# Kernel tuning notes

Measured on AMD Instinct MI355X. Metric: run time of the kernel, lower is better.

Reference implementation:

```python
import jax, jax.numpy as jnp
import numpy as np

N = 50000
IN_C, HID_C, OUT_C = 512, 64, 40
E = 800000

def setup_inputs() -> dict:
    key = jax.random.key(0)
    ks = jax.random.split(key, 6)
    x = jax.random.normal(ks[0], (N, IN_C), dtype=jnp.float32)
    edge_index = jax.random.randint(ks[1], (2, E), 0, N, dtype=jnp.int64)
    # Glorot-style init for GCNConv linear weights, zero bias (PyG default)
    W1 = jax.random.normal(ks[2], (IN_C, HID_C), dtype=jnp.float32) / np.sqrt(IN_C)
    b1 = jnp.zeros((HID_C,), dtype=jnp.float32)
    W2 = jax.random.normal(ks[3], (HID_C, OUT_C), dtype=jnp.float32) / np.sqrt(HID_C)
    b2 = jnp.zeros((OUT_C,), dtype=jnp.float32)
    return {"x": x, "edge_index": edge_index, "W1": W1, "b1": b1, "W2": W2, "b2": b2}

def _gcn_conv(x, src, dst, W, b, n_nodes):
    # Standard GCNConv (self-loops already appended to src/dst):
    # h = x @ W; out[dst] += D^-1/2[src] * D^-1/2[dst] * h[src]; out += b
    h = x @ W
    deg = jnp.zeros((n_nodes,), dtype=h.dtype).at[dst].add(1.0)
    dinv = jnp.where(deg > 0, deg ** -0.5, 0.0)
    norm = dinv[src] * dinv[dst]                       # [E+N]
    msg = h[src] * norm[:, None]                       # gather + scale
    out = jax.ops.segment_sum(msg, dst, num_segments=n_nodes)
    return out + b

def reference(x, edge_index, W1, b1, W2, b2):
    n_nodes = x.shape[0]
    # add self-loops (PyG GCNConv default add_self_loops=True)
    loop = jnp.arange(n_nodes, dtype=edge_index.dtype)
    src = jnp.concatenate([edge_index[0], loop])
    dst = jnp.concatenate([edge_index[1], loop])
    # eval mode: dropout is identity
    h = _gcn_conv(x, src, dst, W1, b1, n_nodes)
    h = jax.nn.relu(h)
    h = _gcn_conv(h, src, dst, W2, b2, n_nodes)
    return jax.nn.softmax(h, axis=-1)
```

## Files before the change

kernel.cpp:

```cpp
#include <hip/hip_runtime.h>
#include <math.h>

#define IN_C 512
#define HID  64
#define OUTC 40

typedef __attribute__((ext_vector_type(8))) short bf16x8;
typedef __attribute__((ext_vector_type(4))) float f32x4;

#define GDEPTH 16

__device__ __forceinline__ ushort f2bf(float f) {
    uint u = __float_as_uint(f);
    u += 0x7FFFu + ((u >> 16) & 1u);
    return (ushort)(u >> 16);
}
__device__ __forceinline__ float bf2f(ushort s) {
    return __uint_as_float(((uint)s) << 16);
}

__device__ __forceinline__ void gl_lds16(const void* g, void* l) {
    __builtin_amdgcn_global_load_lds(
        (const __attribute__((address_space(1))) void*)g,
        (__attribute__((address_space(3))) void*)l,
        16, 0, 0);
}

__global__ void k_zero(int4* __restrict__ p, int n4) {
    int i = blockIdx.x * blockDim.x + threadIdx.x;
    if (i < n4) p[i] = make_int4(0, 0, 0, 0);
}

__global__ void k_histsplit(const int* __restrict__ dst, int E,
                            int* __restrict__ cnt, int* __restrict__ rank,
                            int nbE2,
                            const float* __restrict__ W,
                            ushort* __restrict__ hi, ushort* __restrict__ lo) {
    if (blockIdx.x < (unsigned)nbE2) {
        int i = (blockIdx.x * blockDim.x + threadIdx.x) * 2;
        if (i < E) {
            if (i + 1 < E) {
                int2 d = *(const int2*)&dst[i];
                int r0 = atomicAdd(&cnt[d.x], 1);
                int r1 = atomicAdd(&cnt[d.y], 1);
                *(int2*)&rank[i] = make_int2(r0, r1);
            } else {
                rank[i] = atomicAdd(&cnt[dst[i]], 1);
            }
        }
    } else {
        int i = (blockIdx.x - nbE2) * blockDim.x + threadIdx.x;
        if (i >= HID * IN_C) return;
        int c = i >> 9, k = i & 511;
        float v = W[(size_t)k * HID + c];
        uint ub = __float_as_uint(v);
        uint hb = ub & 0xFFFF0000u;
        float lf = v - __uint_as_float(hb);
        int lb = c * 64 + (k & 31) * 2;
        int pb = lb ^ (((lb >> 6) & 7) << 4);
        int pidx = (k >> 5) * 2048 + (pb >> 1);
        hi[pidx] = (ushort)(ub >> 16);
        lo[pidx] = (ushort)(__float_as_uint(lf) >> 16);
    }
}

__global__ void k_scan1(const int* __restrict__ cnt, int N,
                        int* __restrict__ rowptr, int* __restrict__ bsum) {
    __shared__ int s[256];
    int t = threadIdx.x;
    int i = blockIdx.x * 256 + t;
    int v = (i < N) ? cnt[i] : 0;
    int x = v;
    s[t] = x; __syncthreads();
    #pragma unroll
    for (int o = 1; o < 256; o <<= 1) {
        int y = (t >= o) ? s[t - o] : 0;
        __syncthreads();
        x += y; s[t] = x;
        __syncthreads();
    }
    if (i < N) rowptr[i] = x - v;
    if (t == 255) bsum[blockIdx.x] = x;
}

__global__ void k_scan23(int* __restrict__ rowptr, const int* __restrict__ bsum,
                         const int* __restrict__ cnt, float* __restrict__ dinv,
                         int N, int E, int nb) {
    __shared__ int s[256];
    int t = threadIdx.x;
    int v = (t < nb) ? bsum[t] : 0;
    int x = v;
    s[t] = x; __syncthreads();
    #pragma unroll
    for (int o = 1; o < 256; o <<= 1) {
        int y = (t >= o) ? s[t - o] : 0;
        __syncthreads();
        x += y; s[t] = x;
        __syncthreads();
    }
    int bpre = (blockIdx.x > 0) ? s[blockIdx.x - 1] : 0;
    int i = blockIdx.x * 256 + t;
    if (i < N) {
        rowptr[i] += bpre;
        dinv[i] = rsqrtf(1.0f + (float)cnt[i]);
        if (i == 0) rowptr[N] = E;
    }
}

__global__ __launch_bounds__(256) void k_gemm1fill(
        const float* __restrict__ x,
        const ushort* __restrict__ Bphi, const ushort* __restrict__ Bplo,
        const float* __restrict__ dinv, ushort* __restrict__ h1s,
        int N, int nbG,
        const int* __restrict__ src, const int* __restrict__ dst,
        const int* __restrict__ rank, int E,
        const int* __restrict__ rowptr, int* __restrict__ ssort) {
    __shared__ float  Af[2][2048];
    __shared__ ushort Bh[2][2048], Bl[2][2048];

    if (blockIdx.x >= (unsigned)nbG) {
        int i = ((blockIdx.x - nbG) * blockDim.x + threadIdx.x) * 2;
        if (i >= E) return;
        if (i + 1 < E) {
            int2 d = *(const int2*)&dst[i];
            int2 s = *(const int2*)&src[i];
            int2 r = *(const int2*)&rank[i];
            ssort[rowptr[d.x] + r.x] = s.x;
            ssort[rowptr[d.y] + r.y] = s.y;
        } else {
            ssort[rowptr[dst[i]] + rank[i]] = src[i];
        }
        return;
    }

    int t = threadIdx.x;
    int wid = t >> 6, lane = t & 63;
    int lr = lane & 15, lko = lane >> 4;
    int wm = wid >> 1, wn = wid & 1;
    int row0 = blockIdx.x * 64;

    int p0 = (wid * 64 + lane) * 16;
    int r0l = p0 >> 7;
    int o0 = p0 ^ ((r0l & 7) << 4);
    int g0 = row0 + r0l; if (g0 >= N) g0 = N - 1;
    const char* xsrc0 = (const char*)x + (size_t)g0 * 2048 + (o0 & 127);
    int p1 = p0 + 4096;
    int r1l = p1 >> 7;
    int o1 = p1 ^ ((r1l & 7) << 4);
    int g1 = row0 + r1l; if (g1 >= N) g1 = N - 1;
    const char* xsrc1 = (const char*)x + (size_t)g1 * 2048 + (o1 & 127);
    const char* bsrcH = (const char*)Bphi + (size_t)(wid * 64 + lane) * 16;
    const char* bsrcL = (const char*)Bplo + (size_t)(wid * 64 + lane) * 16;

    f32x4 acc[2][2] = {};

    auto stage = [&](int tile, int b) {
        gl_lds16(xsrc0 + (size_t)tile * 128, (char*)&Af[b][0] + wid * 1024);
        gl_lds16(xsrc1 + (size_t)tile * 128, (char*)&Af[b][0] + 4096 + wid * 1024);
        gl_lds16(bsrcH + (size_t)tile * 4096, (char*)&Bh[b][0] + wid * 1024);
        gl_lds16(bsrcL + (size_t)tile * 4096, (char*)&Bl[b][0] + wid * 1024);
    };
    auto compute = [&](int b) {
        bf16x8 afh[2], afl[2], bfh[2], bfl[2];
        #pragma unroll
        for (int mf = 0; mf < 2; ++mf) {
            int row = wm * 32 + mf * 16 + lr;
            int fi = (row * 32 + lko * 8) ^ ((row & 7) << 2);
            f32x4 a0 = *(const f32x4*)&Af[b][fi];
            f32x4 a1 = *(const f32x4*)&Af[b][fi ^ 4];
            float av[8];
            *(f32x4*)&av[0] = a0;
            *(f32x4*)&av[4] = a1;
            #pragma unroll
            for (int j = 0; j < 8; ++j) {
                uint ub = __float_as_uint(av[j]);
                float hf = __uint_as_float(ub & 0xFFFF0000u);
                float lf = av[j] - hf;
                afh[mf][j] = (short)(ub >> 16);
                afl[mf][j] = (short)(__float_as_uint(lf) >> 16);
            }
        }
        #pragma unroll
        for (int nf = 0; nf < 2; ++nf) {
            int col = wn * 32 + nf * 16 + lr;
            int ci = (col * 32 + lko * 8) ^ ((col & 7) << 3);
            bfh[nf] = *(const bf16x8*)&Bh[b][ci];
            bfl[nf] = *(const bf16x8*)&Bl[b][ci];
        }
        #pragma unroll
        for (int mf = 0; mf < 2; ++mf)
            #pragma unroll
            for (int nf = 0; nf < 2; ++nf) {
                acc[mf][nf] = __builtin_amdgcn_mfma_f32_16x16x32_bf16(afh[mf], bfh[nf], acc[mf][nf], 0, 0, 0);
                acc[mf][nf] = __builtin_amdgcn_mfma_f32_16x16x32_bf16(afl[mf], bfh[nf], acc[mf][nf], 0, 0, 0);
                acc[mf][nf] = __builtin_amdgcn_mfma_f32_16x16x32_bf16(afh[mf], bfl[nf], acc[mf][nf], 0, 0, 0);
            }
    };

    stage(0, 0);
    __syncthreads();

    #pragma unroll
    for (int i = 0; i < 16; ++i) {
        if (i < 15) stage(i + 1, (i + 1) & 1);
        compute(i & 1);
        __syncthreads();
    }

    #pragma unroll
    for (int mf = 0; mf < 2; ++mf)
        #pragma unroll
        for (int r = 0; r < 4; ++r) {
            int orow = row0 + wm * 32 + mf * 16 + lko * 4 + r;
            if (orow < N) {
                float dv = dinv[orow];
                #pragma unroll
                for (int nf = 0; nf < 2; ++nf)
                    h1s[(size_t)orow * HID + wn * 32 + nf * 16 + lr] = f2bf(dv * acc[mf][nf][r]);
            }
        }
}

__global__ __launch_bounds__(256) void k_agg1g2(const ushort* __restrict__ h1s,
                                                const int* __restrict__ rowptr,
                                                const int* __restrict__ ssort,
                                                const float* __restrict__ dinv,
                                                const float* __restrict__ b1,
                                                const float* __restrict__ W2,
                                                ushort* __restrict__ h2s, int N) {
    __shared__ float wl[HID * OUTC];
    int t = threadIdx.x;
    #pragma unroll
    for (int q0 = 0; q0 < 3; ++q0) {
        int q = t + q0 * 256;
        if (q < 640) *(float4*)&wl[q * 4] = *(const float4*)&W2[q * 4];
    }
    __syncthreads();

    int lane = t & 63;
    int wq = t >> 6;
    int lc = lane < OUTC ? lane : 0;
    float bias = b1[lane];
    int nq = (N + 3) >> 2;

    for (int q = blockIdx.x; q < nq; q += gridDim.x) {
        int node = q * 4 + wq;
        if (node >= N) continue;
        float s0 = bf2f(h1s[(size_t)node * HID + lane]);
        float sv[GDEPTH];
        #pragma unroll
        for (int k = 0; k < GDEPTH; ++k) sv[k] = 0.f;
        int eu = __builtin_amdgcn_readfirstlane(rowptr[node]);
        int endu = __builtin_amdgcn_readfirstlane(rowptr[node + 1]);
        for (int e = eu; e < endu; e += GDEPTH) {
            int raw[GDEPTH];
            #pragma unroll
            for (int k = 0; k < GDEPTH; ++k) raw[k] = ssort[e + k];
            #pragma unroll
            for (int k = 0; k < GDEPTH; ++k) {
                int ix = (e + k < endu) ? raw[k] : raw[0];
                float v = bf2f(h1s[(size_t)ix * HID + lane]);
                sv[k] += (e + k < endu) ? v : 0.f;
            }
        }
        float s = s0;
        #pragma unroll
        for (int k = 0; k < GDEPTH; ++k) s += sv[k];
        float dv = dinv[node];
        float a = fmaxf(fmaf(dv, s, bias), 0.0f);
        float acc = 0.f;
        #pragma unroll
        for (int k = 0; k < HID; ++k) {
            float ak = __uint_as_float(__builtin_amdgcn_readlane(__float_as_uint(a), k));
            acc = fmaf(ak, wl[k * OUTC + lc], acc);
        }
        if (lane < OUTC) h2s[(size_t)node * OUTC + lane] = f2bf(dv * acc);
    }
}

__global__ __launch_bounds__(256) void k_agg2(const ushort* __restrict__ h2s,
                                              const int* __restrict__ rowptr,
                                              const int* __restrict__ ssort,
                                              const float* __restrict__ dinv,
                                              const float* __restrict__ b2,
                                              float* __restrict__ out, int N) {
    int lane = threadIdx.x & 63;
    int node = blockIdx.x * 4 + (threadIdx.x >> 6);
    if (node >= N) return;
    bool act = lane < OUTC;
    int lc = act ? lane : 0;
    float s0 = bf2f(h2s[(size_t)node * OUTC + lc]);
    float sv[GDEPTH];
    #pragma unroll
    for (int k = 0; k < GDEPTH; ++k) sv[k] = 0.f;
    int eu = __builtin_amdgcn_readfirstlane(rowptr[node]);
    int endu = __builtin_amdgcn_readfirstlane(rowptr[node + 1]);
    for (int e = eu; e < endu; e += GDEPTH) {
        int raw[GDEPTH];
        #pragma unroll
        for (int k = 0; k < GDEPTH; ++k) raw[k] = ssort[e + k];
        #pragma unroll
        for (int k = 0; k < GDEPTH; ++k) {
            int ix = (e + k < endu) ? raw[k] : raw[0];
            float v = bf2f(h2s[(size_t)ix * OUTC + lc]);
            sv[k] += (e + k < endu) ? v : 0.f;
        }
    }
    float s = s0;
    #pragma unroll
    for (int k = 0; k < GDEPTH; ++k) s += sv[k];
    float v = act ? (dinv[node] * s + b2[lane]) : -INFINITY;
    float m = v;
    #pragma unroll
    for (int o = 32; o; o >>= 1) m = fmaxf(m, __shfl_xor(m, o));
    float p = act ? expf(v - m) : 0.0f;
    float su = p;
    #pragma unroll
    for (int o = 32; o; o >>= 1) su += __shfl_xor(su, o);
    if (act) out[(size_t)node * OUTC + lane] = p / su;
}

static inline size_t alignup(size_t v) { return (v + 255) & ~(size_t)255; }

extern "C" void kernel_launch(void* const* d_in, const int* in_sizes, int n_in,
                              void* d_out, int out_size, void* d_ws, size_t ws_size,
                              hipStream_t stream) {
    const float* x  = (const float*)d_in[0];
    const int*   ei = (const int*)d_in[1];
    const float* W1 = (const float*)d_in[2];
    const float* b1 = (const float*)d_in[3];
    const float* W2 = (const float*)d_in[4];
    const float* b2 = (const float*)d_in[5];

    const int N = in_sizes[0] / IN_C;
    const int E = in_sizes[1] / 2;
    const int* src = ei;
    const int* dst = ei + E;

    char* w = (char*)d_ws;
    int* cnt    = (int*)w;   w += alignup((size_t)N * 4);
    int* rank   = (int*)w;   w += alignup((size_t)E * 4 + 256);
    int* rowptr = (int*)w;   w += alignup((size_t)(N + 1) * 4);
    int* bsum   = (int*)w;   w += alignup(256 * 4);
    int* ssort  = (int*)w;   w += alignup((size_t)E * 4 + 256);
    float* dinv = (float*)w; w += alignup((size_t)N * 4);
    ushort* h1s = (ushort*)w; w += alignup((size_t)N * HID * 2);
    ushort* h2s = (ushort*)w; w += alignup((size_t)N * OUTC * 2);
    ushort* Bphi = (ushort*)w; w += alignup((size_t)HID * IN_C * 2);
    ushort* Bplo = (ushort*)w; w += alignup((size_t)HID * IN_C * 2);

    const int n4 = (N + 3) / 4;
    k_zero<<<(n4 + 255) / 256, 256, 0, stream>>>((int4*)cnt, n4);

    const int nb   = (N + 255) / 256;
    const int nbE2 = (E / 2 + 255) / 256;
    const int nbW  = (HID * IN_C + 255) / 256;
    k_histsplit<<<nbE2 + nbW, 256, 0, stream>>>(dst, E, cnt, rank, nbE2, W1, Bphi, Bplo);
    k_scan1 <<<nb, 256, 0, stream>>>(cnt, N, rowptr, bsum);
    k_scan23<<<nb, 256, 0, stream>>>(rowptr, bsum, cnt, dinv, N, E, nb);

    const int nbG = (N + 63) / 64;
    k_gemm1fill<<<nbG + nbE2, 256, 0, stream>>>(x, Bphi, Bplo, dinv, h1s, N, nbG,
                                                src, dst, rank, E, rowptr, ssort);
    k_agg1g2<<<2048, 256, 0, stream>>>(h1s, rowptr, ssort, dinv, b1, W2, h2s, N);
    k_agg2  <<<(N + 3) / 4, 256, 0, stream>>>(h2s, rowptr, ssort, dinv, b2, (float*)d_out, N);
}
```

Baseline: 143.0 us.

## Split fill from GEMM1 and load full 32-row A tile into LDS upfront

The ssort fill pass is moved out of the fused GEMM launch into its own kernel. The first-layer GEMM now uses 32-row tiles and issues loads for the entire 32x512 fp32 A block into LDS at kernel start, so the K loop only double-buffers the small W1 hi/lo tiles. This issues all x traffic early for more memory-level parallelism, at the cost of 64KB+ of LDS per block, lower occupancy, one extra kernel launch and less per-wave MFMA reuse.

```diff
diff --git a/kernel.cpp b/kernel.cpp
--- a/kernel.cpp
+++ b/kernel.cpp
@@ -107,118 +107,101 @@
     }
 }
 
-__global__ __launch_bounds__(256) void k_gemm1fill(
+__global__ void k_fill(const int* __restrict__ src, const int* __restrict__ dst,
+                       const int* __restrict__ rank, int E,
+                       const int* __restrict__ rowptr, int* __restrict__ ssort) {
+    int i = (blockIdx.x * blockDim.x + threadIdx.x) * 2;
+    if (i >= E) return;
+    if (i + 1 < E) {
+        int2 d = *(const int2*)&dst[i];
+        int2 s = *(const int2*)&src[i];
+        int2 r = *(const int2*)&rank[i];
+        ssort[rowptr[d.x] + r.x] = s.x;
+        ssort[rowptr[d.y] + r.y] = s.y;
+    } else {
+        ssort[rowptr[dst[i]] + rank[i]] = src[i];
+    }
+}
+
+__global__ __launch_bounds__(256) void k_gemm1(
         const float* __restrict__ x,
         const ushort* __restrict__ Bphi, const ushort* __restrict__ Bplo,
-        const float* __restrict__ dinv, ushort* __restrict__ h1s,
-        int N, int nbG,
-        const int* __restrict__ src, const int* __restrict__ dst,
-        const int* __restrict__ rank, int E,
-        const int* __restrict__ rowptr, int* __restrict__ ssort) {
-    __shared__ float  Af[2][2048];
+        const float* __restrict__ dinv, ushort* __restrict__ h1s, int N) {
+    __shared__ float  Af[32 * 512];
     __shared__ ushort Bh[2][2048], Bl[2][2048];
-
-    if (blockIdx.x >= (unsigned)nbG) {
-        int i = ((blockIdx.x - nbG) * blockDim.x + threadIdx.x) * 2;
-        if (i >= E) return;
-        if (i + 1 < E) {
-            int2 d = *(const int2*)&dst[i];
-            int2 s = *(const int2*)&src[i];
-            int2 r = *(const int2*)&rank[i];
-            ssort[rowptr[d.x] + r.x] = s.x;
-            ssort[rowptr[d.y] + r.y] = s.y;
-        } else {
-            ssort[rowptr[dst[i]] + rank[i]] = src[i];
-        }
-        return;
-    }
 
     int t = threadIdx.x;
     int wid = t >> 6, lane = t & 63;
     int lr = lane & 15, lko = lane >> 4;
     int wm = wid >> 1, wn = wid & 1;
-    int row0 = blockIdx.x * 64;
-
-    int p0 = (wid * 64 + lane) * 16;
-    int r0l = p0 >> 7;
-    int o0 = p0 ^ ((r0l & 7) << 4);
-    int g0 = row0 + r0l; if (g0 >= N) g0 = N - 1;
-    const char* xsrc0 = (const char*)x + (size_t)g0 * 2048 + (o0 & 127);
-    int p1 = p0 + 4096;
-    int r1l = p1 >> 7;
-    int o1 = p1 ^ ((r1l & 7) << 4);
-    int g1 = row0 + r1l; if (g1 >= N) g1 = N - 1;
-    const char* xsrc1 = (const char*)x + (size_t)g1 * 2048 + (o1 & 127);
-    const char* bsrcH = (const char*)Bphi + (size_t)(wid * 64 + lane) * 16;
-    const char* bsrcL = (const char*)Bplo + (size_t)(wid * 64 + lane) * 16;
-
-    f32x4 acc[2][2] = {};
-
-    auto stage = [&](int tile, int b) {
-        gl_lds16(xsrc0 + (size_t)tile * 128, (char*)&Af[b][0] + wid * 1024);
-        gl_lds16(xsrc1 + (size_t)tile * 128, (char*)&Af[b][0] + 4096 + wid * 1024);
-        gl_lds16(bsrcH + (size_t)tile * 4096, (char*)&Bh[b][0] + wid * 1024);
-        gl_lds16(bsrcL + (size_t)tile * 4096, (char*)&Bl[b][0] + wid * 1024);
-    };
-    auto compute = [&](int b) {
-        bf16x8 afh[2], afl[2], bfh[2], bfl[2];
-        #pragma unroll
-        for (int mf = 0; mf < 2; ++mf) {
-            int row = wm * 32 + mf * 16 + lr;
-            int fi = (row * 32 + lko * 8) ^ ((row & 7) << 2);
-            f32x4 a0 = *(const f32x4*)&Af[b][fi];
-            f32x4 a1 = *(const f32x4*)&Af[b][fi ^ 4];
-            float av[8];
-            *(f32x4*)&av[0] = a0;
-            *(f32x4*)&av[4] = a1;
-            #pragma unroll
-            for (int j = 0; j < 8; ++j) {
-                uint ub = __float_as_uint(av[j]);
-                float hf = __uint_as_float(ub & 0xFFFF0000u);
-                float lf = av[j] - hf;
-                afh[mf][j] = (short)(ub >> 16);
-                afl[mf][j] = (short)(__float_as_uint(lf) >> 16);
-            }
-        }
+    int row0 = blockIdx.x * 32;
+
+    const char* xb = (const char*)x;
+    #pragma unroll
+    for (int j = 0; j < 16; ++j) {
+        int p = t * 16 + j * 4096;
+        int row = p >> 11;
+        int o = (p & 2047) ^ ((row & 7) << 4);
+        int grow = row0 + row; if (grow >= N) grow = N - 1;
+        gl_lds16(xb + (size_t)grow * 2048 + o, (char*)Af + j * 4096 + wid * 1024);
+    }
+    const char* bsrcH = (const char*)Bphi + (size_t)t * 16;
+    const char* bsrcL = (const char*)Bplo + (size_t)t * 16;
+    gl_lds16(bsrcH, (char*)&Bh[0][0] + wid * 1024);
+    gl_lds16(bsrcL, (char*)&Bl[0][0] + wid * 1024);
+    __syncthreads();
+
+    f32x4 acc[2] = {};
+
+    #pragma unroll
+    for (int i = 0; i < 16; ++i) {
+        if (i < 15) {
+            gl_lds16(bsrcH + (size_t)(i + 1) * 4096, (char*)&Bh[(i + 1) & 1][0] + wid * 1024);
+            gl_lds16(bsrcL + (size_t)(i + 1) * 4096, (char*)&Bl[(i + 1) & 1][0] + wid * 1024);
+        }
+        int row = wm * 16 + lr;
+        int fi = (row * 512 + i * 32 + lko * 8) ^ ((row & 7) << 2);
+        f32x4 a0 = *(const f32x4*)&Af[fi];
+        f32x4 a1 = *(const f32x4*)&Af[fi ^ 4];
+        float av[8];
+        *(f32x4*)&av[0] = a0;
+        *(f32x4*)&av[4] = a1;
+        bf16x8 ahi, alo;
+        #pragma unroll
+        for (int j = 0; j < 8; ++j) {
+            uint ub = __float_as_uint(av[j]);
+            float hf = __uint_as_float(ub & 0xFFFF0000u);
+            float lf = av[j] - hf;
+            ahi[j] = (short)(ub >> 16);
+            alo[j] = (short)(__float_as_uint(lf) >> 16);
+        }
+        bf16x8 bfh[2], bfl[2];
         #pragma unroll
         for (int nf = 0; nf < 2; ++nf) {
             int col = wn * 32 + nf * 16 + lr;
             int ci = (col * 32 + lko * 8) ^ ((col & 7) << 3);
-            bfh[nf] = *(const bf16x8*)&Bh[b][ci];
-            bfl[nf] = *(const bf16x8*)&Bl[b][ci];
-        }
-        #pragma unroll
-        for (int mf = 0; mf < 2; ++mf)
+            bfh[nf] = *(const bf16x8*)&Bh[i & 1][ci];
+            bfl[nf] = *(const bf16x8*)&Bl[i & 1][ci];
+        }
+        #pragma unroll
+        for (int nf = 0; nf < 2; ++nf) {
+            acc[nf] = __builtin_amdgcn_mfma_f32_16x16x32_bf16(ahi, bfh[nf], acc[nf], 0, 0, 0);
+            acc[nf] = __builtin_amdgcn_mfma_f32_16x16x32_bf16(alo, bfh[nf], acc[nf], 0, 0, 0);
+            acc[nf] = __builtin_amdgcn_mfma_f32_16x16x32_bf16(ahi, bfl[nf], acc[nf], 0, 0, 0);
+        }
+        __syncthreads();
+    }
+
+    #pragma unroll
+    for (int r = 0; r < 4; ++r) {
+        int orow = row0 + wm * 16 + lko * 4 + r;
+        if (orow < N) {
+            float dv = dinv[orow];
             #pragma unroll
-            for (int nf = 0; nf < 2; ++nf) {
-                acc[mf][nf] = __builtin_amdgcn_mfma_f32_16x16x32_bf16(afh[mf], bfh[nf], acc[mf][nf], 0, 0, 0);
-                acc[mf][nf] = __builtin_amdgcn_mfma_f32_16x16x32_bf16(afl[mf], bfh[nf], acc[mf][nf], 0, 0, 0);
-                acc[mf][nf] = __builtin_amdgcn_mfma_f32_16x16x32_bf16(afh[mf], bfl[nf], acc[mf][nf], 0, 0, 0);
-            }
-    };
-
-    stage(0, 0);
-    __syncthreads();
-
-    #pragma unroll
-    for (int i = 0; i < 16; ++i) {
-        if (i < 15) stage(i + 1, (i + 1) & 1);
-        compute(i & 1);
-        __syncthreads();
-    }
-
-    #pragma unroll
-    for (int mf = 0; mf < 2; ++mf)
-        #pragma unroll
-        for (int r = 0; r < 4; ++r) {
-            int orow = row0 + wm * 32 + mf * 16 + lko * 4 + r;
-            if (orow < N) {
-                float dv = dinv[orow];
-                #pragma unroll
-                for (int nf = 0; nf < 2; ++nf)
-                    h1s[(size_t)orow * HID + wn * 32 + nf * 16 + lr] = f2bf(dv * acc[mf][nf][r]);
-            }
-        }
+            for (int nf = 0; nf < 2; ++nf)
+                h1s[(size_t)orow * HID + wn * 32 + nf * 16 + lr] = f2bf(dv * acc[nf][r]);
+        }
+    }
 }
 
 __global__ __launch_bounds__(256) void k_agg1g2(const ushort* __restrict__ h1s,
@@ -358,10 +341,9 @@
     k_histsplit<<<nbE2 + nbW, 256, 0, stream>>>(dst, E, cnt, rank, nbE2, W1, Bphi, Bplo);
     k_scan1 <<<nb, 256, 0, stream>>>(cnt, N, rowptr, bsum);
     k_scan23<<<nb, 256, 0, stream>>>(rowptr, bsum, cnt, dinv, N, E, nb);
-
-    const int nbG = (N + 63) / 64;
-    k_gemm1fill<<<nbG + nbE2, 256, 0, stream>>>(x, Bphi, Bplo, dinv, h1s, N, nbG,
-                                                src, dst, rank, E, rowptr, ssort);
+    k_fill  <<<nbE2, 256, 0, stream>>>(src, dst, rank, E, rowptr, ssort);
+
+    k_gemm1 <<<(N + 31) / 32, 256, 0, stream>>>(x, Bphi, Bplo, dinv, h1s, N);
     k_agg1g2<<<2048, 256, 0, stream>>>(h1s, rowptr, ssort, dinv, b1, W2, h2s, N);
     k_agg2  <<<(N + 3) / 4, 256, 0, stream>>>(h2s, rowptr, ssort, dinv, b2, (float*)d_out, N);
 }
```

Measured after the change: 172.6 us. +20.7%, slower.

## Split layer-1 aggregation into two 32-channel halves for cache locality, separate GEMM2

Applied to the files above, without the earlier changes.

The first GEMM now writes the hidden features as two separate 32-channel arrays. Aggregation runs in two passes, one per half, so each gathered working set is half the size and more likely to stay in L2/MALL. The aggregated activation is written to a new buffer, and a separate kernel applies W2. This adds an extra kernel launch, an extra pass over the edge list, and an extra read and write of the activation buffer.

```diff
diff --git a/kernel.cpp b/kernel.cpp
--- a/kernel.cpp
+++ b/kernel.cpp
@@ -110,7 +110,8 @@
 __global__ __launch_bounds__(256) void k_gemm1fill(
         const float* __restrict__ x,
         const ushort* __restrict__ Bphi, const ushort* __restrict__ Bplo,
-        const float* __restrict__ dinv, ushort* __restrict__ h1s,
+        const float* __restrict__ dinv,
+        ushort* __restrict__ h1a, ushort* __restrict__ h1b,
         int N, int nbG,
         const int* __restrict__ src, const int* __restrict__ dst,
         const int* __restrict__ rank, int E,
@@ -207,6 +208,7 @@
         __syncthreads();
     }
 
+    ushort* hb = wn ? h1b : h1a;
     #pragma unroll
     for (int mf = 0; mf < 2; ++mf)
         #pragma unroll
@@ -216,16 +218,47 @@
                 float dv = dinv[orow];
                 #pragma unroll
                 for (int nf = 0; nf < 2; ++nf)
-                    h1s[(size_t)orow * HID + wn * 32 + nf * 16 + lr] = f2bf(dv * acc[mf][nf][r]);
+                    hb[(size_t)orow * 32 + nf * 16 + lr] = f2bf(dv * acc[mf][nf][r]);
             }
         }
 }
 
-__global__ __launch_bounds__(256) void k_agg1g2(const ushort* __restrict__ h1s,
-                                                const int* __restrict__ rowptr,
-                                                const int* __restrict__ ssort,
+__global__ __launch_bounds__(256) void k_aggh(const ushort* __restrict__ h1x,
+                                              const int* __restrict__ rowptr,
+                                              const int* __restrict__ ssort,
+                                              const float* __restrict__ dinv,
+                                              const float* __restrict__ b1,
+                                              ushort* __restrict__ a1f,
+                                              int N, int half) {
+    int t = blockIdx.x * blockDim.x + threadIdx.x;
+    int node = t >> 5;
+    int ch = t & 31;
+    if (node >= N) return;
+    float s0 = bf2f(h1x[(size_t)node * 32 + ch]);
+    float sv[GDEPTH];
+    #pragma unroll
+    for (int k = 0; k < GDEPTH; ++k) sv[k] = 0.f;
+    int elo = rowptr[node], ehi = rowptr[node + 1];
+    for (int e = elo; e < ehi; e += GDEPTH) {
+        int raw[GDEPTH];
+        #pragma unroll
+        for (int k = 0; k < GDEPTH; ++k) raw[k] = ssort[e + k];
+        #pragma unroll
+        for (int k = 0; k < GDEPTH; ++k) {
+            int ix = (e + k < ehi) ? raw[k] : raw[0];
+            float v = bf2f(h1x[(size_t)ix * 32 + ch]);
+            sv[k] += (e + k < ehi) ? v : 0.f;
+        }
+    }
+    float s = s0;
+    #pragma unroll
+    for (int k = 0; k < GDEPTH; ++k) s += sv[k];
+    float a = fmaxf(fmaf(dinv[node], s, b1[half * 32 + ch]), 0.0f);
+    __builtin_nontemporal_store(f2bf(a), &a1f[(size_t)node * 64 + half * 32 + ch]);
+}
+
+__global__ __launch_bounds__(256) void k_gemm2b(const ushort* __restrict__ a1f,
                                                 const float* __restrict__ dinv,
-                                                const float* __restrict__ b1,
                                                 const float* __restrict__ W2,
                                                 ushort* __restrict__ h2s, int N) {
     __shared__ float wl[HID * OUTC];
@@ -236,46 +269,18 @@
         if (q < 640) *(float4*)&wl[q * 4] = *(const float4*)&W2[q * 4];
     }
     __syncthreads();
-
     int lane = t & 63;
-    int wq = t >> 6;
+    int node = blockIdx.x * 4 + (t >> 6);
+    if (node >= N) return;
     int lc = lane < OUTC ? lane : 0;
-    float bias = b1[lane];
-    int nq = (N + 3) >> 2;
-
-    for (int q = blockIdx.x; q < nq; q += gridDim.x) {
-        int node = q * 4 + wq;
-        if (node >= N) continue;
-        float s0 = bf2f(h1s[(size_t)node * HID + lane]);
-        float sv[GDEPTH];
-        #pragma unroll
-        for (int k = 0; k < GDEPTH; ++k) sv[k] = 0.f;
-        int eu = __builtin_amdgcn_readfirstlane(rowptr[node]);
-        int endu = __builtin_amdgcn_readfirstlane(rowptr[node + 1]);
-        for (int e = eu; e < endu; e += GDEPTH) {
-            int raw[GDEPTH];
-            #pragma unroll
-            for (int k = 0; k < GDEPTH; ++k) raw[k] = ssort[e + k];
-            #pragma unroll
-            for (int k = 0; k < GDEPTH; ++k) {
-                int ix = (e + k < endu) ? raw[k] : raw[0];
-                float v = bf2f(h1s[(size_t)ix * HID + lane]);
-                sv[k] += (e + k < endu) ? v : 0.f;
-            }
-        }
-        float s = s0;
-        #pragma unroll
-        for (int k = 0; k < GDEPTH; ++k) s += sv[k];
-        float dv = dinv[node];
-        float a = fmaxf(fmaf(dv, s, bias), 0.0f);
-        float acc = 0.f;
-        #pragma unroll
-        for (int k = 0; k < HID; ++k) {
-            float ak = __uint_as_float(__builtin_amdgcn_readlane(__float_as_uint(a), k));
-            acc = fmaf(ak, wl[k * OUTC + lc], acc);
-        }
-        if (lane < OUTC) h2s[(size_t)node * OUTC + lane] = f2bf(dv * acc);
-    }
+    float a = bf2f(a1f[(size_t)node * 64 + lane]);
+    float acc = 0.f;
+    #pragma unroll
+    for (int k = 0; k < HID; ++k) {
+        float ak = __uint_as_float(__builtin_amdgcn_readlane(__float_as_uint(a), k));
+        acc = fmaf(ak, wl[k * OUTC + lc], acc);
+    }
+    if (lane < OUTC) h2s[(size_t)node * OUTC + lane] = f2bf(dinv[node] * acc);
 }
 
 __global__ __launch_bounds__(256) void k_agg2(const ushort* __restrict__ h2s,
@@ -344,7 +349,9 @@
     int* bsum   = (int*)w;   w += alignup(256 * 4);
     int* ssort  = (int*)w;   w += alignup((size_t)E * 4 + 256);
     float* dinv = (float*)w; w += alignup((size_t)N * 4);
-    ushort* h1s = (ushort*)w; w += alignup((size_t)N * HID * 2);
+    ushort* h1a = (ushort*)w; w += alignup((size_t)N * 32 * 2);
+    ushort* h1b = (ushort*)w; w += alignup((size_t)N * 32 * 2);
+    ushort* a1f = (ushort*)w; w += alignup((size_t)N * HID * 2);
     ushort* h2s = (ushort*)w; w += alignup((size_t)N * OUTC * 2);
     ushort* Bphi = (ushort*)w; w += alignup((size_t)HID * IN_C * 2);
     ushort* Bplo = (ushort*)w; w += alignup((size_t)HID * IN_C * 2);
@@ -360,8 +367,11 @@
     k_scan23<<<nb, 256, 0, stream>>>(rowptr, bsum, cnt, dinv, N, E, nb);
 
     const int nbG = (N + 63) / 64;
-    k_gemm1fill<<<nbG + nbE2, 256, 0, stream>>>(x, Bphi, Bplo, dinv, h1s, N, nbG,
+    k_gemm1fill<<<nbG + nbE2, 256, 0, stream>>>(x, Bphi, Bplo, dinv, h1a, h1b, N, nbG,
                                                 src, dst, rank, E, rowptr, ssort);
-    k_agg1g2<<<2048, 256, 0, stream>>>(h1s, rowptr, ssort, dinv, b1, W2, h2s, N);
-    k_agg2  <<<(N + 3) / 4, 256, 0, stream>>>(h2s, rowptr, ssort, dinv, b2, (float*)d_out, N);
-}
+    const int nbA = ((size_t)N * 32 + 255) / 256;
+    k_aggh <<<nbA, 256, 0, stream>>>(h1a, rowptr, ssort, dinv, b1, a1f, N, 0);
+    k_aggh <<<nbA, 256, 0, stream>>>(h1b, rowptr, ssort, dinv, b1, a1f, N, 1);
+    k_gemm2b<<<(N + 3) / 4, 256, 0, stream>>>(a1f, dinv, W2, h2s, N);
+    k_agg2 <<<(N + 3) / 4, 256, 0, stream>>>(h2s, rowptr, ssort, dinv, b2, (float*)d_out, N);
+}
```

New measurement: 160.7 us. 1.12x slower.
